# Performance work log

Hardware: AMD Instinct MI355X
Metric: run time of the kernel (lower is better)

## Reference

```python
import jax, jax.numpy as jnp
import numpy as np

HIDDEN = 1024
FFN = 2048
NUM_EXPERTS = 16
JITTER_EPS = 0.01


def setup_inputs() -> dict:
    key = jax.random.key(0)
    k1, k2, k3, k4 = jax.random.split(key, 4)
    hidden_states = jax.random.normal(k1, (4, 2048, HIDDEN), dtype=jnp.float32)
    gate_weight = jax.random.normal(k2, (NUM_EXPERTS, HIDDEN), dtype=jnp.float32) * 0.02
    # gate_up_weights[e, :FFN] = w1 (gate proj), [FFN:] = w3 (up proj)
    gate_up_weights = jax.random.normal(k3, (NUM_EXPERTS, 2 * FFN, HIDDEN), dtype=jnp.float32) * 0.02
    down_weights = jax.random.normal(k4, (NUM_EXPERTS, HIDDEN, FFN), dtype=jnp.float32) * 0.02
    return {
        'hidden_states': hidden_states,
        'gate_weight': gate_weight,
        'gate_up_weights': gate_up_weights,
        'down_weights': down_weights,
    }


def sparsemixer(scores, jitter_eps):
    # top-1 selection with jitter mask
    m1 = jnp.max(scores, axis=-1, keepdims=True)              # [T,1]
    ind1 = jnp.argmax(scores, axis=-1, keepdims=True)         # [T,1]
    factor1 = jnp.maximum(jnp.abs(scores), m1)
    mask1 = (m1 - scores) / factor1 > 2.0 * jitter_eps
    gates1 = jax.nn.softmax(jnp.where(mask1, -jnp.inf, scores), axis=-1)
    w1 = jnp.take_along_axis(gates1, ind1, axis=-1)           # [T,1]

    # mask out top-1, select top-2
    top1_onehot = jax.nn.one_hot(ind1[:, 0], scores.shape[-1], dtype=bool)
    masked_scores = jnp.where(top1_onehot, -jnp.inf, scores)
    m2 = jnp.max(masked_scores, axis=-1, keepdims=True)
    ind2 = jnp.argmax(masked_scores, axis=-1, keepdims=True)
    factor2 = jnp.maximum(jnp.abs(scores), m2)
    mask2 = (m2 - scores) / factor2 > 2.0 * jitter_eps
    gates2 = jax.nn.softmax(jnp.where(mask2, -jnp.inf, masked_scores), axis=-1)
    w2 = jnp.take_along_axis(gates2, ind2, axis=-1)           # [T,1]

    multipliers = jnp.concatenate([w1, w2], axis=-1)          # [T,2]
    experts = jnp.concatenate([ind1, ind2], axis=-1)          # [T,2] int
    return multipliers, experts


def fused_moe(x, gate_up_weights, down_weights, routing_weights, selected_experts):
    # x: [T,H], gate_up: [E,2F,H], down: [E,H,F]
    E = gate_up_weights.shape[0]
    ffn = down_weights.shape[2]
    # combine[t,e] = sum_k routing_weights[t,k] * (selected[t,k]==e)
    onehot = jax.nn.one_hot(selected_experts, E, dtype=x.dtype)     # [T,2,E]
    combine = jnp.einsum('tk,tke->te', routing_weights, onehot)     # [T,E]
    out = jnp.zeros_like(x)
    for e in range(E):
        gu = x @ gate_up_weights[e].T                                # [T,2F]
        h = jax.nn.silu(gu[:, :ffn]) * gu[:, ffn:]                   # [T,F]
        out = out + combine[:, e:e + 1] * (h @ down_weights[e].T)    # [T,H]
    return out


def reference(hidden_states, gate_weight, gate_up_weights, down_weights):
    B, S, H = hidden_states.shape
    x = hidden_states.reshape(-1, H)                         # [T,H]
    router_logits = x @ gate_weight.T                        # [T,E]
    routing_weights, selected_experts = sparsemixer(router_logits, JITTER_EPS)
    out = fused_moe(x, gate_up_weights, down_weights, routing_weights, selected_experts)
    return out.reshape(B, S, H), router_logits
```

## Files before the change

### kernel.cpp

```cpp
#include <hip/hip_runtime.h>
#include <hip/hip_bf16.h>
#include <math.h>

#define T_TOKENS 8192
#define HID 1024
#define FFN 2048
#define NEXP 16
#define NPAIR (2*T_TOKENS)
#define TM 128
#define MAXTILES 144

typedef short bf16x8 __attribute__((ext_vector_type(8)));
typedef float f32x4 __attribute__((ext_vector_type(4)));

static const size_t HPACK_OFF = 0;
static const size_t HPACK_SZ  = (size_t)MAXTILES * 32 * 16384;
static const size_t GPACK_OFF = HPACK_OFF + HPACK_SZ;
static const size_t GPACK_SZ  = (size_t)16 * 64 * 16 * 8192;
static const size_t DPACK_OFF = GPACK_OFF + GPACK_SZ;
static const size_t DPACK_SZ  = (size_t)16 * 16 * 32 * 8192;
static const size_t APACK_OFF = DPACK_OFF + DPACK_SZ;
static const size_t APACK_SZ  = (size_t)MAXTILES * 16 * 16384;
static const size_t WTK_OFF   = APACK_OFF + APACK_SZ;
static const size_t ETK_OFF   = WTK_OFF  + (size_t)NPAIR*4;
static const size_t RANK_OFF  = ETK_OFF  + (size_t)NPAIR*4;
static const size_t LIST_OFF  = RANK_OFF + (size_t)NPAIR*4;
static const size_t CNT_OFF   = LIST_OFF + (size_t)NPAIR*4;
static const size_t OFFS_OFF  = CNT_OFF  + 64;
static const size_t TEXP_OFF  = OFFS_OFF + 128;
static const size_t TSEG_OFF  = TEXP_OFF + (size_t)MAXTILES*4;
static const size_t HDR_OFF   = TSEG_OFF + (size_t)MAXTILES*4;

__device__ __forceinline__ unsigned short f2bf(float f) {
  union { float f; unsigned u; } v; v.f = f;
  unsigned r = v.u + 0x7fff + ((v.u >> 16) & 1);
  return (unsigned short)(r >> 16);
}

__device__ __forceinline__ bf16x8 pack8(float4 a, float4 b) {
  bf16x8 r;
  r[0]=(short)f2bf(a.x); r[1]=(short)f2bf(a.y); r[2]=(short)f2bf(a.z); r[3]=(short)f2bf(a.w);
  r[4]=(short)f2bf(b.x); r[5]=(short)f2bf(b.y); r[6]=(short)f2bf(b.z); r[7]=(short)f2bf(b.w);
  return r;
}

__device__ __forceinline__ void ld16(const unsigned short* g, unsigned short* l) {
  __builtin_amdgcn_global_load_lds((const __attribute__((address_space(1))) void*)g,
                                   (__attribute__((address_space(3))) void*)l, 16, 0, 0);
}

__global__ __launch_bounds__(256) void k_pack(const float* __restrict__ src, unsigned short* __restrict__ dst,
                                              int nbcnt, int kbcnt, int kdim) {
  int e = blockIdx.z, nb = blockIdx.y, kb = blockIdx.x;
  __shared__ unsigned short tile[4096];
  int tid = threadIdx.x;
  int n = tid >> 2, ks = (tid & 3) * 16;
  const float* s = src + ((size_t)((e*nbcnt + nb)*64 + n))*kdim + kb*64 + ks;
  float4 f0 = *(const float4*)(s);
  float4 f1 = *(const float4*)(s + 4);
  float4 f2 = *(const float4*)(s + 8);
  float4 f3 = *(const float4*)(s + 12);
  int kkc0 = ks >> 3;
  *(bf16x8*)&tile[(kkc0*64 + n)*8]     = pack8(f0, f1);
  *(bf16x8*)&tile[((kkc0+1)*64 + n)*8] = pack8(f2, f3);
  __syncthreads();
  unsigned short* d = dst + ((size_t)(e*nbcnt + nb)*kbcnt + kb)*4096 + tid*16;
  *(bf16x8*)(d)     = *(const bf16x8*)&tile[tid*16];
  *(bf16x8*)(d + 8) = *(const bf16x8*)&tile[tid*16 + 8];
}

__global__ __launch_bounds__(256) void k_logits(const float* __restrict__ x,
                                                const float* __restrict__ gw,
                                                float* __restrict__ logits) {
  int tid = threadIdx.x;
  int wave = tid >> 6, lane = tid & 63;
  int t = blockIdx.x * 4 + wave;
  const float* xp = x + (size_t)t * HID;
  float acc[NEXP];
  #pragma unroll
  for (int e = 0; e < NEXP; e++) acc[e] = 0.f;
  for (int i = lane; i < HID; i += 64) {
    float xv = xp[i];
    #pragma unroll
    for (int e = 0; e < NEXP; e++) acc[e] += xv * gw[e*HID + i];
  }
  float mine = 0.f;
  #pragma unroll
  for (int e = 0; e < NEXP; e++) {
    float v = acc[e];
    #pragma unroll
    for (int o = 32; o > 0; o >>= 1) v += __shfl_xor(v, o, 64);
    if (lane == e) mine = v;
  }
  if (lane < NEXP) logits[(size_t)t*NEXP + lane] = mine;
}

__global__ __launch_bounds__(256) void k_route(const float* __restrict__ logits,
                                               float* __restrict__ wtk, int* __restrict__ etk,
                                               int* __restrict__ rank, int* __restrict__ counts) {
  int t = blockIdx.x*256 + threadIdx.x;
  if (t >= T_TOKENS) return;
  float s[NEXP];
  const float* lp = logits + (size_t)t*NEXP;
  #pragma unroll
  for (int e = 0; e < NEXP; e++) s[e] = lp[e];

  float m1 = s[0]; int i1 = 0;
  #pragma unroll
  for (int e = 1; e < NEXP; e++) if (s[e] > m1) { m1 = s[e]; i1 = e; }
  float sum1 = 0.f;
  #pragma unroll
  for (int e = 0; e < NEXP; e++) {
    float f = fmaxf(fabsf(s[e]), m1);
    if (!((m1 - s[e]) > 0.02f*f)) sum1 += expf(s[e]-m1);
  }
  float m2 = -INFINITY; int i2 = 0;
  #pragma unroll
  for (int e = 0; e < NEXP; e++) if (e != i1 && s[e] > m2) { m2 = s[e]; i2 = e; }
  float sum2 = 0.f;
  #pragma unroll
  for (int e = 0; e < NEXP; e++) {
    if (e == i1) continue;
    float f = fmaxf(fabsf(s[e]), m2);
    if (!((m2 - s[e]) > 0.02f*f)) sum2 += expf(s[e]-m2);
  }
  wtk[t*2]   = 1.f/sum1;
  wtk[t*2+1] = 1.f/sum2;
  etk[t*2]   = i1;
  etk[t*2+1] = i2;
  rank[t*2]   = atomicAdd(&counts[i1], 1);
  rank[t*2+1] = atomicAdd(&counts[i2], 1);
}

__global__ void k_scan(const int* __restrict__ counts, int* __restrict__ offsets,
                       int* __restrict__ texp, int* __restrict__ tseg, int* __restrict__ hdr) {
  if (threadIdx.x != 0 || blockIdx.x != 0) return;
  int off = 0, nt = 0;
  for (int e = 0; e < NEXP; e++) {
    offsets[e] = off;
    int c = counts[e];
    int tiles = (c + TM - 1)/TM;
    for (int i = 0; i < tiles; i++) { texp[nt] = e; tseg[nt] = i; nt++; }
    off += c;
  }
  offsets[NEXP] = off;
  hdr[0] = nt;
}

__global__ __launch_bounds__(256) void k_scatter(const int* __restrict__ etk,
                                                 const int* __restrict__ rank,
                                                 const int* __restrict__ offsets,
                                                 int* __restrict__ list) {
  int p = blockIdx.x*256 + threadIdx.x;
  if (p >= NPAIR) return;
  int e = etk[p];
  list[offsets[e] + rank[p]] = p;
}

__global__ __launch_bounds__(256) void k_agather(const float* __restrict__ x,
                                                 const int* __restrict__ list,
                                                 const int* __restrict__ counts,
                                                 const int* __restrict__ offsets,
                                                 const int* __restrict__ texp,
                                                 const int* __restrict__ tseg,
                                                 const int* __restrict__ hdr,
                                                 unsigned short* __restrict__ apack) {
  int by = blockIdx.x;
  if (by >= hdr[0]) return;
  int e = texp[by];
  int m0 = tseg[by]*TM;
  int seg0 = offsets[e];
  int cnt = counts[e];
  __shared__ int toks[TM];
  int tid = threadIdx.x;
  if (tid < TM) toks[tid] = list[seg0 + min(m0 + tid, cnt-1)] >> 1;
  __syncthreads();
  #pragma unroll 4
  for (int it = 0; it < 64; ++it) {
    int flat = it*256 + tid;
    int kb = flat >> 10;
    int i  = flat & 1023;
    int kkc = i >> 7, row = i & 127;
    const float* s = x + (size_t)toks[row]*HID + kb*64 + kkc*8;
    float4 f0 = *(const float4*)(s);
    float4 f1 = *(const float4*)(s + 4);
    *(bf16x8*)(apack + ((size_t)(by*16 + kb))*8192 + (size_t)i*8) = pack8(f0, f1);
  }
}

__global__ __launch_bounds__(256,4) void k_gateup(const unsigned short* __restrict__ apack,
                                                  const unsigned short* __restrict__ gpack,
                                                  const float* __restrict__ wtk,
                                                  const int* __restrict__ list,
                                                  const int* __restrict__ counts,
                                                  const int* __restrict__ offsets,
                                                  const int* __restrict__ texp,
                                                  const int* __restrict__ tseg,
                                                  const int* __restrict__ hdr,
                                                  unsigned short* __restrict__ hpack) {
  int fb = blockIdx.x;
  int by = blockIdx.y;
  if (by >= hdr[0]) return;
  int e = texp[by];
  int m0 = tseg[by]*TM;
  int seg0 = offsets[e];
  int cnt = counts[e];
  int rows = min(TM, cnt - m0);

  __shared__ __align__(16) unsigned short A_lds[2][4096];
  __shared__ __align__(16) unsigned short Bg_lds[2][2048];
  __shared__ __align__(16) unsigned short Bu_lds[2][2048];

  int tid = threadIdx.x;
  int wid = tid >> 6, lane = tid & 63;
  int wr = wid >> 1, wc = wid & 1;
  int c4 = lane >> 4, r16 = lane & 15;

  const unsigned short* gA = apack + (size_t)by * 131072;
  const unsigned short* gG = gpack + ((size_t)(e*64 + fb))      * 65536;
  const unsigned short* gU = gpack + ((size_t)(e*64 + 32 + fb)) * 65536;

  f32x4 accg[4][2] = {};
  f32x4 accu[4][2] = {};

  auto STAGE = [&](int buf, int kb) {
    #pragma unroll
    for (int s = 0; s < 4; ++s) {
      int i = wid*4 + s;
      if (i < 8) {
        ld16(gA + (size_t)kb*4096 + i*512 + lane*8, &A_lds[buf][i*512]);
      } else if (i < 12) {
        int j = i - 8;
        ld16(gG + (size_t)kb*2048 + j*512 + lane*8, &Bg_lds[buf][j*512]);
      } else {
        int j = i - 12;
        ld16(gU + (size_t)kb*2048 + j*512 + lane*8, &Bu_lds[buf][j*512]);
      }
    }
  };

  auto COMPUTE = [&](int buf) {
    bf16x8 a[4], bg[2], bu[2];
    #pragma unroll
    for (int sm = 0; sm < 4; ++sm)
      a[sm] = *(const bf16x8*)&A_lds[buf][(c4*128 + wr*64 + sm*16 + r16)*8];
    #pragma unroll
    for (int sn = 0; sn < 2; ++sn) {
      bg[sn] = *(const bf16x8*)&Bg_lds[buf][(c4*64 + wc*32 + sn*16 + r16)*8];
      bu[sn] = *(const bf16x8*)&Bu_lds[buf][(c4*64 + wc*32 + sn*16 + r16)*8];
    }
    #pragma unroll
    for (int sm = 0; sm < 4; ++sm)
      #pragma unroll
      for (int sn = 0; sn < 2; ++sn) {
        accg[sm][sn] = __builtin_amdgcn_mfma_f32_16x16x32_bf16(a[sm], bg[sn], accg[sm][sn], 0, 0, 0);
        accu[sm][sn] = __builtin_amdgcn_mfma_f32_16x16x32_bf16(a[sm], bu[sn], accu[sm][sn], 0, 0, 0);
      }
  };

  STAGE(0, 0);
  __syncthreads();
  int cur = 0;
  for (int kb = 0; kb < 31; ++kb) {
    STAGE(cur ^ 1, kb + 1);
    COMPUTE(cur);
    __syncthreads();
    cur ^= 1;
  }
  COMPUTE(cur);
  __syncthreads();

  unsigned short* scr = &A_lds[0][0];
  #pragma unroll
  for (int sm = 0; sm < 4; ++sm) {
    #pragma unroll
    for (int j = 0; j < 4; ++j) {
      int row = wr*64 + sm*16 + (lane>>4)*4 + j;
      float w = (row < rows) ? wtk[list[seg0 + m0 + row]] : 0.f;
      #pragma unroll
      for (int sn = 0; sn < 2; ++sn) {
        int col = wc*32 + sn*16 + (lane & 15);
        float g = accg[sm][sn][j];
        float u = accu[sm][sn][j];
        float hv = g / (1.f + __expf(-g)) * u * w;
        scr[((col>>3)*128 + row)*8 + (col&7)] = f2bf(hv);
      }
    }
  }
  __syncthreads();
  unsigned short* dst = hpack + ((size_t)(by*32 + fb))*8192 + tid*32;
  const unsigned short* srcl = scr + tid*32;
  #pragma unroll
  for (int q = 0; q < 4; ++q)
    *(bf16x8*)(dst + q*8) = *(const bf16x8*)(srcl + q*8);
}

__global__ __launch_bounds__(256,4) void k_down(const unsigned short* __restrict__ hpack,
                                                const unsigned short* __restrict__ dpack,
                                                const int* __restrict__ counts,
                                                const int* __restrict__ texp,
                                                const int* __restrict__ tseg,
                                                const int* __restrict__ offsets,
                                                const int* __restrict__ hdr,
                                                float* __restrict__ ydown) {
  int nb = blockIdx.x;
  int by = blockIdx.y;
  if (by >= hdr[0]) return;
  int e = texp[by];
  int m0 = tseg[by]*TM;
  int seg0 = offsets[e];
  int cnt = counts[e];
  int rows = min(TM, cnt - m0);

  __shared__ __align__(16) unsigned short A_lds[2][4096];
  __shared__ __align__(16) unsigned short B_lds[2][4096];

  int tid = threadIdx.x;
  int wid = tid >> 6, lane = tid & 63;
  int wr = wid >> 1, wc = wid & 1;
  int c4 = lane >> 4, r16 = lane & 15;

  const unsigned short* hA = hpack + (size_t)by * 262144;

  f32x4 acc[4][4] = {};

  auto STAGE = [&](int buf, int kb) {
    #pragma unroll
    for (int s = 0; s < 4; ++s) {
      int i = wid*4 + s;
      if (i < 8) {
        ld16(hA + (size_t)kb*4096 + i*512 + lane*8, &A_lds[buf][i*512]);
      } else {
        int i2 = i - 8;
        int p = i2 >> 2, j = i2 & 3;
        ld16(dpack + (((size_t)(e*16 + nb*2 + p))*32 + (kb>>1))*4096 + (kb&1)*2048 + j*512 + lane*8,
             &B_lds[buf][p*2048 + j*512]);
      }
    }
  };

  auto COMPUTE = [&](int buf) {
    bf16x8 a[4], b[4];
    #pragma unroll
    for (int sm = 0; sm < 4; ++sm)
      a[sm] = *(const bf16x8*)&A_lds[buf][(c4*128 + wr*64 + sm*16 + r16)*8];
    #pragma unroll
    for (int sn = 0; sn < 4; ++sn) {
      int col = wc*64 + sn*16 + r16;
      b[sn] = *(const bf16x8*)&B_lds[buf][(col>>6)*2048 + (c4*64 + (col&63))*8];
    }
    #pragma unroll
    for (int sm = 0; sm < 4; ++sm)
      #pragma unroll
      for (int sn = 0; sn < 4; ++sn)
        acc[sm][sn] = __builtin_amdgcn_mfma_f32_16x16x32_bf16(a[sm], b[sn], acc[sm][sn], 0, 0, 0);
  };

  STAGE(0, 0);
  __syncthreads();
  int cur = 0;
  for (int kb = 0; kb < 63; ++kb) {
    STAGE(cur ^ 1, kb + 1);
    COMPUTE(cur);
    __syncthreads();
    cur ^= 1;
  }
  COMPUTE(cur);

  #pragma unroll
  for (int sm = 0; sm < 4; ++sm) {
    #pragma unroll
    for (int j = 0; j < 4; ++j) {
      int row = wr*64 + sm*16 + (lane>>4)*4 + j;
      if (row < rows) {
        size_t slot = (size_t)(seg0 + m0 + row);
        #pragma unroll
        for (int sn = 0; sn < 4; ++sn) {
          int col = nb*128 + wc*64 + sn*16 + r16;
          ydown[slot*HID + col] = acc[sm][sn][j];
        }
      }
    }
  }
}

__global__ __launch_bounds__(256) void k_final(const float* __restrict__ ydown,
                                               const int* __restrict__ etk,
                                               const int* __restrict__ rank,
                                               const int* __restrict__ offsets,
                                               float* __restrict__ out) {
  int t = blockIdx.x;
  int c = threadIdx.x;
  int p0 = t*2, p1 = t*2 + 1;
  int s0 = offsets[etk[p0]] + rank[p0];
  int s1 = offsets[etk[p1]] + rank[p1];
  float4 a = *(const float4*)(ydown + (size_t)s0*HID + c*4);
  float4 b = *(const float4*)(ydown + (size_t)s1*HID + c*4);
  float4 r; r.x = a.x+b.x; r.y = a.y+b.y; r.z = a.z+b.z; r.w = a.w+b.w;
  *(float4*)(out + (size_t)t*HID + c*4) = r;
}

extern "C" void kernel_launch(void* const* d_in, const int* in_sizes, int n_in,
                              void* d_out, int out_size, void* d_ws, size_t ws_size,
                              hipStream_t stream) {
  const float* x   = (const float*)d_in[0];
  const float* gw  = (const float*)d_in[1];
  const float* gup = (const float*)d_in[2];
  const float* dwn = (const float*)d_in[3];

  float* out = (float*)d_out;
  float* logits = out + (size_t)T_TOKENS*HID;

  char* ws = (char*)d_ws;
  unsigned short* hpack = (unsigned short*)(ws + HPACK_OFF);
  unsigned short* gpack = (unsigned short*)(ws + GPACK_OFF);
  unsigned short* dpack = (unsigned short*)(ws + DPACK_OFF);
  unsigned short* apack = (unsigned short*)(ws + APACK_OFF);
  float* ydown = (float*)(ws + GPACK_OFF);
  float* wtk   = (float*)(ws + WTK_OFF);
  int* etk     = (int*)(ws + ETK_OFF);
  int* rank    = (int*)(ws + RANK_OFF);
  int* list    = (int*)(ws + LIST_OFF);
  int* counts  = (int*)(ws + CNT_OFF);
  int* offsets = (int*)(ws + OFFS_OFF);
  int* texp    = (int*)(ws + TEXP_OFF);
  int* tseg    = (int*)(ws + TSEG_OFF);
  int* hdr     = (int*)(ws + HDR_OFF);

  hipMemsetAsync(counts, 0, 64, stream);

  k_logits<<<T_TOKENS/4, 256, 0, stream>>>(x, gw, logits);
  k_route<<<T_TOKENS/256, 256, 0, stream>>>(logits, wtk, etk, rank, counts);
  k_scan<<<1, 64, 0, stream>>>(counts, offsets, texp, tseg, hdr);
  k_scatter<<<NPAIR/256, 256, 0, stream>>>(etk, rank, offsets, list);
  k_agather<<<MAXTILES, 256, 0, stream>>>(x, list, counts, offsets, texp, tseg, hdr, apack);

  {
    dim3 g(16, 64, NEXP);
    k_pack<<<g, 256, 0, stream>>>(gup, gpack, 64, 16, HID);
  }
  {
    dim3 g(32, 16, NEXP);
    k_pack<<<g, 256, 0, stream>>>(dwn, dpack, 16, 32, FFN);
  }

  dim3 g3(32, MAXTILES);
  k_gateup<<<g3, 256, 0, stream>>>(apack, gpack, wtk, list, counts, offsets, texp, tseg, hdr, hpack);

  dim3 g4(8, MAXTILES);
  k_down<<<g4, 256, 0, stream>>>(hpack, dpack, counts, texp, tseg, offsets, hdr, ydown);

  k_final<<<T_TOKENS, 256, 0, stream>>>(ydown, etk, rank, offsets, out);
}
```

Baseline: 562.8 us.

## Give each wave private LDS buffers and drop block barriers in MoE GEMM loops

In both the gate-up and down GEMM kernels, each wave now loads its own A and B sub-tiles into a private double-buffered LDS region. It then synchronises with explicit vmcnt/lgkmcnt waits instead of a block-wide __syncthreads every k-step. This removes barrier stalls between waves and lets loads and MFMA overlap per wave. The cost is duplicated global/LDS traffic for shared operands, since A is loaded once per column-wave and B once per row-wave. LDS per block grows to 64KB and launch bounds drop to 2 blocks per CU.

New measurement: 606.4 us. 1.08x slower.

```diff
diff --git a/kernel.cpp b/kernel.cpp
--- a/kernel.cpp
+++ b/kernel.cpp
@@ -48,6 +48,10 @@
   __builtin_amdgcn_global_load_lds((const __attribute__((address_space(1))) void*)g,
                                    (__attribute__((address_space(3))) void*)l, 16, 0, 0);
 }
+
+#define WAITV8 do { asm volatile("s_waitcnt vmcnt(8)" ::: "memory"); __builtin_amdgcn_sched_barrier(0); } while (0)
+#define WAITV0 do { asm volatile("s_waitcnt vmcnt(0)" ::: "memory"); __builtin_amdgcn_sched_barrier(0); } while (0)
+#define WAITL0 do { asm volatile("s_waitcnt lgkmcnt(0)" ::: "memory"); __builtin_amdgcn_sched_barrier(0); } while (0)
 
 __global__ __launch_bounds__(256) void k_pack(const float* __restrict__ src, unsigned short* __restrict__ dst,
                                               int nbcnt, int kbcnt, int kdim) {
@@ -188,7 +192,7 @@
   }
 }
 
-__global__ __launch_bounds__(256,4) void k_gateup(const unsigned short* __restrict__ apack,
+__global__ __launch_bounds__(256,2) void k_gateup(const unsigned short* __restrict__ apack,
                                                   const unsigned short* __restrict__ gpack,
                                                   const float* __restrict__ wtk,
                                                   const int* __restrict__ list,
@@ -207,14 +211,13 @@
   int cnt = counts[e];
   int rows = min(TM, cnt - m0);
 
-  __shared__ __align__(16) unsigned short A_lds[2][4096];
-  __shared__ __align__(16) unsigned short Bg_lds[2][2048];
-  __shared__ __align__(16) unsigned short Bu_lds[2][2048];
+  __shared__ __align__(16) unsigned short lds_[4][2][4096];
 
   int tid = threadIdx.x;
   int wid = tid >> 6, lane = tid & 63;
   int wr = wid >> 1, wc = wid & 1;
   int c4 = lane >> 4, r16 = lane & 15;
+  int lh = lane >> 5, l31 = lane & 31;
 
   const unsigned short* gA = apack + (size_t)by * 131072;
   const unsigned short* gG = gpack + ((size_t)(e*64 + fb))      * 65536;
@@ -223,31 +226,32 @@
   f32x4 accg[4][2] = {};
   f32x4 accu[4][2] = {};
 
-  auto STAGE = [&](int buf, int kb) {
-    #pragma unroll
-    for (int s = 0; s < 4; ++s) {
-      int i = wid*4 + s;
-      if (i < 8) {
-        ld16(gA + (size_t)kb*4096 + i*512 + lane*8, &A_lds[buf][i*512]);
-      } else if (i < 12) {
-        int j = i - 8;
-        ld16(gG + (size_t)kb*2048 + j*512 + lane*8, &Bg_lds[buf][j*512]);
-      } else {
-        int j = i - 12;
-        ld16(gU + (size_t)kb*2048 + j*512 + lane*8, &Bu_lds[buf][j*512]);
-      }
+  unsigned short* wb0 = &lds_[wid][0][0];
+  unsigned short* wb1 = &lds_[wid][1][0];
+
+  auto STAGE = [&](unsigned short* base, int s) {
+    int kb = s >> 1, hf = s & 1;
+    const unsigned short* As = gA + (size_t)kb*8192 + (size_t)(hf*4*128 + wr*64 + lane)*8;
+    #pragma unroll
+    for (int c = 0; c < 4; ++c) ld16(As + c*1024, base + c*512);
+    const unsigned short* Gs = gG + (size_t)kb*4096 + (size_t)((hf*4 + lh)*64 + wc*32 + l31)*8;
+    const unsigned short* Us = gU + (size_t)kb*4096 + (size_t)((hf*4 + lh)*64 + wc*32 + l31)*8;
+    #pragma unroll
+    for (int c = 0; c < 2; ++c) {
+      ld16(Gs + c*1024, base + 2048 + c*512);
+      ld16(Us + c*1024, base + 3072 + c*512);
     }
   };
 
-  auto COMPUTE = [&](int buf) {
+  auto COMPUTE = [&](const unsigned short* base) {
     bf16x8 a[4], bg[2], bu[2];
     #pragma unroll
     for (int sm = 0; sm < 4; ++sm)
-      a[sm] = *(const bf16x8*)&A_lds[buf][(c4*128 + wr*64 + sm*16 + r16)*8];
+      a[sm] = *(const bf16x8*)&base[(c4*64 + sm*16 + r16)*8];
     #pragma unroll
     for (int sn = 0; sn < 2; ++sn) {
-      bg[sn] = *(const bf16x8*)&Bg_lds[buf][(c4*64 + wc*32 + sn*16 + r16)*8];
-      bu[sn] = *(const bf16x8*)&Bu_lds[buf][(c4*64 + wc*32 + sn*16 + r16)*8];
+      bg[sn] = *(const bf16x8*)&base[2048 + (c4*32 + sn*16 + r16)*8];
+      bu[sn] = *(const bf16x8*)&base[3072 + (c4*32 + sn*16 + r16)*8];
     }
     #pragma unroll
     for (int sm = 0; sm < 4; ++sm)
@@ -258,19 +262,20 @@
       }
   };
 
-  STAGE(0, 0);
+  STAGE(wb0, 0);
+  STAGE(wb1, 1);
+  for (int s = 0; s < 31; ++s) {
+    unsigned short* cb = (s & 1) ? wb1 : wb0;
+    WAITV8;
+    COMPUTE(cb);
+    WAITL0;
+    if (s < 30) STAGE(cb, s + 2);
+  }
+  WAITV0;
+  COMPUTE(wb1);
   __syncthreads();
-  int cur = 0;
-  for (int kb = 0; kb < 31; ++kb) {
-    STAGE(cur ^ 1, kb + 1);
-    COMPUTE(cur);
-    __syncthreads();
-    cur ^= 1;
-  }
-  COMPUTE(cur);
-  __syncthreads();
-
-  unsigned short* scr = &A_lds[0][0];
+
+  unsigned short* scr = &lds_[0][0][0];
   #pragma unroll
   for (int sm = 0; sm < 4; ++sm) {
     #pragma unroll
@@ -295,7 +300,7 @@
     *(bf16x8*)(dst + q*8) = *(const bf16x8*)(srcl + q*8);
 }
 
-__global__ __launch_bounds__(256,4) void k_down(const unsigned short* __restrict__ hpack,
+__global__ __launch_bounds__(256,2) void k_down(const unsigned short* __restrict__ hpack,
                                                 const unsigned short* __restrict__ dpack,
                                                 const int* __restrict__ counts,
                                                 const int* __restrict__ texp,
@@ -312,8 +317,7 @@
   int cnt = counts[e];
   int rows = min(TM, cnt - m0);
 
-  __shared__ __align__(16) unsigned short A_lds[2][4096];
-  __shared__ __align__(16) unsigned short B_lds[2][4096];
+  __shared__ __align__(16) unsigned short lds_[4][2][4096];
 
   int tid = threadIdx.x;
   int wid = tid >> 6, lane = tid & 63;
@@ -321,34 +325,31 @@
   int c4 = lane >> 4, r16 = lane & 15;
 
   const unsigned short* hA = hpack + (size_t)by * 262144;
+  const unsigned short* dB = dpack + ((size_t)(e*16 + nb*2 + wc)) * 131072;
 
   f32x4 acc[4][4] = {};
 
-  auto STAGE = [&](int buf, int kb) {
-    #pragma unroll
-    for (int s = 0; s < 4; ++s) {
-      int i = wid*4 + s;
-      if (i < 8) {
-        ld16(hA + (size_t)kb*4096 + i*512 + lane*8, &A_lds[buf][i*512]);
-      } else {
-        int i2 = i - 8;
-        int p = i2 >> 2, j = i2 & 3;
-        ld16(dpack + (((size_t)(e*16 + nb*2 + p))*32 + (kb>>1))*4096 + (kb&1)*2048 + j*512 + lane*8,
-             &B_lds[buf][p*2048 + j*512]);
-      }
-    }
+  unsigned short* wb0 = &lds_[wid][0][0];
+  unsigned short* wb1 = &lds_[wid][1][0];
+
+  auto STAGE = [&](unsigned short* base, int s) {
+    int kb = s >> 1, hf = s & 1;
+    const unsigned short* As = hA + (size_t)kb*8192 + (size_t)(hf*4*128 + wr*64 + lane)*8;
+    #pragma unroll
+    for (int c = 0; c < 4; ++c) ld16(As + c*1024, base + c*512);
+    const unsigned short* Bs = dB + (size_t)kb*4096 + (size_t)(hf*4*64 + lane)*8;
+    #pragma unroll
+    for (int c = 0; c < 4; ++c) ld16(Bs + c*512, base + 2048 + c*512);
   };
 
-  auto COMPUTE = [&](int buf) {
+  auto COMPUTE = [&](const unsigned short* base) {
     bf16x8 a[4], b[4];
     #pragma unroll
     for (int sm = 0; sm < 4; ++sm)
-      a[sm] = *(const bf16x8*)&A_lds[buf][(c4*128 + wr*64 + sm*16 + r16)*8];
-    #pragma unroll
-    for (int sn = 0; sn < 4; ++sn) {
-      int col = wc*64 + sn*16 + r16;
-      b[sn] = *(const bf16x8*)&B_lds[buf][(col>>6)*2048 + (c4*64 + (col&63))*8];
-    }
+      a[sm] = *(const bf16x8*)&base[(c4*64 + sm*16 + r16)*8];
+    #pragma unroll
+    for (int sn = 0; sn < 4; ++sn)
+      b[sn] = *(const bf16x8*)&base[2048 + (c4*64 + sn*16 + r16)*8];
     #pragma unroll
     for (int sm = 0; sm < 4; ++sm)
       #pragma unroll
@@ -356,16 +357,17 @@
         acc[sm][sn] = __builtin_amdgcn_mfma_f32_16x16x32_bf16(a[sm], b[sn], acc[sm][sn], 0, 0, 0);
   };
 
-  STAGE(0, 0);
-  __syncthreads();
-  int cur = 0;
-  for (int kb = 0; kb < 63; ++kb) {
-    STAGE(cur ^ 1, kb + 1);
-    COMPUTE(cur);
-    __syncthreads();
-    cur ^= 1;
-  }
-  COMPUTE(cur);
+  STAGE(wb0, 0);
+  STAGE(wb1, 1);
+  for (int s = 0; s < 63; ++s) {
+    unsigned short* cb = (s & 1) ? wb1 : wb0;
+    WAITV8;
+    COMPUTE(cb);
+    WAITL0;
+    if (s < 62) STAGE(cb, s + 2);
+  }
+  WAITV0;
+  COMPUTE(wb1);
 
   #pragma unroll
   for (int sm = 0; sm < 4; ++sm) {
```

## Fuse weight packing into gather and gateup launches, restructure GEMM prefetch pipeline

Applied to the files above, without the earlier changes.

The gate/up weight pack is merged with the activation gather into one launch. The down-weight pack is appended as extra blocks of the gateup kernel, so its packing overlaps with gateup compute. Both GEMM main loops now issue two stages ahead and use explicit vmcnt/lgkmcnt waits with raw barriers in place of __syncthreads, overlapping global-to-LDS loads with MFMA work. The cost is a more fragile hand-counted wait scheme and weight packing that shares launches with compute.

Result: faster. 508.8 us (-9.6%).

```diff
diff --git a/kernel.cpp b/kernel.cpp
--- a/kernel.cpp
+++ b/kernel.cpp
@@ -49,10 +49,14 @@
                                    (__attribute__((address_space(3))) void*)l, 16, 0, 0);
 }
 
-__global__ __launch_bounds__(256) void k_pack(const float* __restrict__ src, unsigned short* __restrict__ dst,
-                                              int nbcnt, int kbcnt, int kdim) {
-  int e = blockIdx.z, nb = blockIdx.y, kb = blockIdx.x;
-  __shared__ unsigned short tile[4096];
+#define WAITV4 do { asm volatile("s_waitcnt vmcnt(4)" ::: "memory"); } while (0)
+#define WAITV0 do { asm volatile("s_waitcnt vmcnt(0)" ::: "memory"); } while (0)
+#define WAITL0 do { asm volatile("s_waitcnt lgkmcnt(0)" ::: "memory"); __builtin_amdgcn_sched_barrier(0); } while (0)
+#define XBAR   do { __builtin_amdgcn_s_barrier(); __builtin_amdgcn_sched_barrier(0); } while (0)
+
+__device__ __forceinline__ void pack_body(const float* __restrict__ src, unsigned short* __restrict__ dst,
+                                          int e, int nb, int kb, int nbcnt, int kbcnt, int kdim,
+                                          unsigned short* tile ) {
   int tid = threadIdx.x;
   int n = tid >> 2, ks = (tid & 3) * 16;
   const float* s = src + ((size_t)((e*nbcnt + nb)*64 + n))*kdim + kb*64 + ks;
@@ -157,21 +161,30 @@
   list[offsets[e] + rank[p]] = p;
 }
 
-__global__ __launch_bounds__(256) void k_agather(const float* __restrict__ x,
-                                                 const int* __restrict__ list,
-                                                 const int* __restrict__ counts,
-                                                 const int* __restrict__ offsets,
-                                                 const int* __restrict__ texp,
-                                                 const int* __restrict__ tseg,
-                                                 const int* __restrict__ hdr,
-                                                 unsigned short* __restrict__ apack) {
-  int by = blockIdx.x;
+__global__ __launch_bounds__(256) void k_prep(const float* __restrict__ gup,
+                                              unsigned short* __restrict__ gpack,
+                                              const float* __restrict__ x,
+                                              const int* __restrict__ list,
+                                              const int* __restrict__ counts,
+                                              const int* __restrict__ offsets,
+                                              const int* __restrict__ texp,
+                                              const int* __restrict__ tseg,
+                                              const int* __restrict__ hdr,
+                                              unsigned short* __restrict__ apack) {
+  __shared__ __align__(16) unsigned short tile[4096];
+  int bid = blockIdx.x;
+  if (bid < 16384) {
+    int kb = bid & 15, nb = (bid >> 4) & 63, e = bid >> 10;
+    pack_body(gup, gpack, e, nb, kb, 64, 16, HID, tile);
+    return;
+  }
+  int by = bid - 16384;
   if (by >= hdr[0]) return;
   int e = texp[by];
   int m0 = tseg[by]*TM;
   int seg0 = offsets[e];
   int cnt = counts[e];
-  __shared__ int toks[TM];
+  int* toks = (int*)tile;
   int tid = threadIdx.x;
   if (tid < TM) toks[tid] = list[seg0 + min(m0 + tid, cnt-1)] >> 1;
   __syncthreads();
@@ -190,6 +203,8 @@
 
 __global__ __launch_bounds__(256,4) void k_gateup(const unsigned short* __restrict__ apack,
                                                   const unsigned short* __restrict__ gpack,
+                                                  const float* __restrict__ dwn,
+                                                  unsigned short* __restrict__ dpack,
                                                   const float* __restrict__ wtk,
                                                   const int* __restrict__ list,
                                                   const int* __restrict__ counts,
@@ -198,18 +213,23 @@
                                                   const int* __restrict__ tseg,
                                                   const int* __restrict__ hdr,
                                                   unsigned short* __restrict__ hpack) {
-  int fb = blockIdx.x;
-  int by = blockIdx.y;
+  __shared__ __align__(16) unsigned short A_lds[2][4096];
+  __shared__ __align__(16) unsigned short Bg_lds[2][2048];
+  __shared__ __align__(16) unsigned short Bu_lds[2][2048];
+  int bid = blockIdx.x;
+  if (bid >= 4608) {
+    int p = bid - 4608;
+    pack_body(dwn, dpack, p >> 9, (p >> 5) & 15, p & 31, 16, 32, FFN, &A_lds[0][0]);
+    return;
+  }
+  int fb = bid & 31;
+  int by = bid >> 5;
   if (by >= hdr[0]) return;
   int e = texp[by];
   int m0 = tseg[by]*TM;
   int seg0 = offsets[e];
   int cnt = counts[e];
   int rows = min(TM, cnt - m0);
-
-  __shared__ __align__(16) unsigned short A_lds[2][4096];
-  __shared__ __align__(16) unsigned short Bg_lds[2][2048];
-  __shared__ __align__(16) unsigned short Bu_lds[2][2048];
 
   int tid = threadIdx.x;
   int wid = tid >> 6, lane = tid & 63;
@@ -259,14 +279,16 @@
   };
 
   STAGE(0, 0);
-  __syncthreads();
+  STAGE(1, 1);
   int cur = 0;
   for (int kb = 0; kb < 31; ++kb) {
-    STAGE(cur ^ 1, kb + 1);
+    WAITV4; XBAR;
     COMPUTE(cur);
-    __syncthreads();
+    WAITL0; XBAR;
+    if (kb < 30) STAGE(cur, kb + 2);
     cur ^= 1;
   }
+  WAITV0; XBAR;
   COMPUTE(cur);
   __syncthreads();
 
@@ -357,14 +379,16 @@
   };
 
   STAGE(0, 0);
-  __syncthreads();
+  STAGE(1, 1);
   int cur = 0;
   for (int kb = 0; kb < 63; ++kb) {
-    STAGE(cur ^ 1, kb + 1);
+    WAITV4; XBAR;
     COMPUTE(cur);
-    __syncthreads();
+    WAITL0; XBAR;
+    if (kb < 62) STAGE(cur, kb + 2);
     cur ^= 1;
   }
+  WAITV0; XBAR;
   COMPUTE(cur);
 
   #pragma unroll
@@ -433,19 +457,11 @@
   k_route<<<T_TOKENS/256, 256, 0, stream>>>(logits, wtk, etk, rank, counts);
   k_scan<<<1, 64, 0, stream>>>(counts, offsets, texp, tseg, hdr);
   k_scatter<<<NPAIR/256, 256, 0, stream>>>(etk, rank, offsets, list);
-  k_agather<<<MAXTILES, 256, 0, stream>>>(x, list, counts, offsets, texp, tseg, hdr, apack);
-
-  {
-    dim3 g(16, 64, NEXP);
-    k_pack<<<g, 256, 0, stream>>>(gup, gpack, 64, 16, HID);
-  }
-  {
-    dim3 g(32, 16, NEXP);
-    k_pack<<<g, 256, 0, stream>>>(dwn, dpack, 16, 32, FFN);
-  }
-
-  dim3 g3(32, MAXTILES);
-  k_gateup<<<g3, 256, 0, stream>>>(apack, gpack, wtk, list, counts, offsets, texp, tseg, hdr, hpack);
+
+  k_prep<<<16384 + MAXTILES, 256, 0, stream>>>(gup, gpack, x, list, counts, offsets, texp, tseg, hdr, apack);
+
+  k_gateup<<<4608 + 8192, 256, 0, stream>>>(apack, gpack, dwn, dpack, wtk, list, counts, offsets,
+                                            texp, tseg, hdr, hpack);
 
   dim3 g4(8, MAXTILES);
   k_down<<<g4, 256, 0, stream>>>(hpack, dpack, counts, texp, tseg, offsets, hdr, ydown);
```
